# Kernel tuning notes

Measured on AMD Instinct MI355X. Metric: run time of the kernel, lower is better.

## Reference

```python
import jax, jax.numpy as jnp
import numpy as np

VOCAB, EMB, HID = 32000, 256, 512
B, S = 4, 512


def setup_inputs() -> dict:
    key = jax.random.key(0)
    ks = jax.random.split(key, 8)
    sc_e = 1.0  # torch nn.Embedding default: N(0,1)
    k_lstm = 1.0 / np.sqrt(HID)
    k_lin = 1.0 / np.sqrt(HID)
    emb = jax.random.normal(ks[0], (VOCAB, EMB), dtype=jnp.float32) * sc_e
    emb = emb.at[0].set(0.0)  # padding_idx=0 row is zero
    w_ih = jax.random.uniform(ks[1], (4 * HID, EMB), minval=-k_lstm, maxval=k_lstm)
    w_hh = jax.random.uniform(ks[2], (4 * HID, HID), minval=-k_lstm, maxval=k_lstm)
    b_ih = jax.random.uniform(ks[3], (4 * HID,), minval=-k_lstm, maxval=k_lstm)
    b_hh = jax.random.uniform(ks[4], (4 * HID,), minval=-k_lstm, maxval=k_lstm)
    W = jax.random.uniform(ks[5], (VOCAB, HID), minval=-k_lin, maxval=k_lin)
    b = jax.random.uniform(ks[6], (VOCAB,), minval=-k_lin, maxval=k_lin)
    batch = jax.random.randint(ks[7], (B, S), 0, VOCAB, dtype=jnp.int64 if jax.config.jax_enable_x64 else jnp.int32)
    return {"batch": batch, "emb": emb, "w_ih": w_ih, "w_hh": w_hh,
            "b_ih": b_ih, "b_hh": b_hh, "W": W, "b": b}


def _lstm(x, w_ih, w_hh, b_ih, b_hh):
    # x: [B, S, E]; torch gate order i, f, g, o; h0 = c0 = 0
    H = w_hh.shape[1]
    bsz = x.shape[0]
    xp = jnp.einsum('bse,ge->bsg', x, w_ih) + b_ih + b_hh  # [B,S,4H]
    xp = jnp.swapaxes(xp, 0, 1)  # [S,B,4H]

    def step(carry, xt):
        h, c = carry
        g = xt + h @ w_hh.T
        i, f, gg, o = jnp.split(g, 4, axis=-1)
        i, f, o = jax.nn.sigmoid(i), jax.nn.sigmoid(f), jax.nn.sigmoid(o)
        c = f * c + i * jnp.tanh(gg)
        h = o * jnp.tanh(c)
        return (h, c), h

    h0 = jnp.zeros((bsz, H), x.dtype)
    _, hs = jax.lax.scan(step, (h0, h0), xp)
    return jnp.swapaxes(hs, 0, 1)  # [B,S,H]


def reference(batch, emb, w_ih, w_hh, b_ih, b_hh, W, b):
    embeds = emb[batch]                               # [B,S,E]
    lstm_out = _lstm(embeds, w_ih, w_hh, b_ih, b_hh)  # [B,S,H]
    logits = jnp.einsum('bsh,vh->bsv', lstm_out, W) + b
    scores = jax.nn.log_softmax(logits, axis=2)       # [B,S,V]
    # Faithful to torch: contiguous view (row-major reinterpretation)
    V = W.shape[0]
    bsz = batch.shape[0]
    scores2 = scores.reshape(-1, V, bsz)              # [S,V,B]
    tgt2 = batch.reshape(-1, bsz)                     # [S,B]
    picked = jnp.take_along_axis(scores2, tgt2[:, None, :], axis=1)[:, 0, :]
    return -jnp.mean(picked)
```

## Files before the change

kernel.cpp:

```cpp
#include <hip/hip_runtime.h>
#include <hip/hip_bf16.h>
#include <math.h>

#define VOCAB 32000
#define EMB   256
#define HID   512
#define BB    4
#define SS    512
#define G4H   2048
#define BS    2048

typedef unsigned int   u32;
typedef unsigned short u16;
using short8 = __attribute__((ext_vector_type(8))) short;
using f32x4  = __attribute__((ext_vector_type(4))) float;

#define OFF_HSB  8192000ull
#define OFF_HW   8716288ull
#define OFF_SUM  8722432ull

__device__ inline unsigned packbf(float a, float b) {
    unsigned ua = __float_as_uint(a), ub = __float_as_uint(b);
    ua += 0x7fffu + ((ua >> 16) & 1u);
    ub += 0x7fffu + ((ub >> 16) & 1u);
    return (ua >> 16) | (ub & 0xffff0000u);
}

__device__ inline float lo16(unsigned w) { return __uint_as_float(w << 16); }
__device__ inline float hi16(unsigned w) { return __uint_as_float(w & 0xffff0000u); }

__device__ inline float fast_tanh(float x) {
    return 1.f - 2.f / (__expf(2.f * x) + 1.f);
}

#define GLOAD_LDS16(gp, lp) __builtin_amdgcn_global_load_lds( \
    (const __attribute__((address_space(1))) void*)(gp),      \
    (__attribute__((address_space(3))) void*)(lp), 16, 0, 0)

__global__ __launch_bounds__(256) void k_embed_xp(
    const int* __restrict__ batch, const float* __restrict__ emb,
    const float* __restrict__ w_ih, const float* __restrict__ b_ih,
    const float* __restrict__ b_hh, float* __restrict__ xp)
{
    __shared__ float Asl[16 * 64];
    __shared__ float Bsl[16 * 64];
    const int tid = threadIdx.x;
    const int bs0 = blockIdx.x * 64;
    const int g0  = blockIdx.y * 64;
    const int m  = tid & 63;
    const int kg = tid >> 6;
    const int tok = batch[bs0 + m];
    const float* arow = emb + (size_t)tok * EMB;
    const float* brow = w_ih + (size_t)(g0 + m) * EMB;
    const int tm = tid >> 4;
    const int tv = tid & 15;

    float acc[4][4] = {};
    for (int k0 = 0; k0 < EMB; k0 += 16) {
        float4 a4 = *(const float4*)(arow + k0 + kg * 4);
        float4 b4 = *(const float4*)(brow + k0 + kg * 4);
        __syncthreads();
        const int kb = kg * 4;
        Asl[(kb + 0) * 64 + m] = a4.x;
        Asl[(kb + 1) * 64 + m] = a4.y;
        Asl[(kb + 2) * 64 + m] = a4.z;
        Asl[(kb + 3) * 64 + m] = a4.w;
        Bsl[(kb + 0) * 64 + m] = b4.x;
        Bsl[(kb + 1) * 64 + m] = b4.y;
        Bsl[(kb + 2) * 64 + m] = b4.z;
        Bsl[(kb + 3) * 64 + m] = b4.w;
        __syncthreads();
#pragma unroll
        for (int k = 0; k < 16; ++k) {
            float4 av = *(const float4*)&Asl[k * 64 + tm * 4];
            float4 bv = *(const float4*)&Bsl[k * 64 + tv * 4];
            float a[4] = {av.x, av.y, av.z, av.w};
            float bb[4] = {bv.x, bv.y, bv.z, bv.w};
#pragma unroll
            for (int i = 0; i < 4; ++i)
#pragma unroll
                for (int j = 0; j < 4; ++j)
                    acc[i][j] += a[i] * bb[j];
        }
    }
    float bsum[4];
#pragma unroll
    for (int j = 0; j < 4; ++j) {
        int g = g0 + tv * 4 + j;
        bsum[j] = b_ih[g] + b_hh[g];
    }
    const int cg = g0 + tv * 4;
    const int gg = cg >> 9;
    const int jj = cg & 511;
    const int sl = jj >> 5;
    const int li = jj & 31;
#pragma unroll
    for (int i = 0; i < 4; ++i) {
        int row = bs0 + tm * 4 + i;
        int cch = row >> 9, tt = row & 511;
        float4 o;
        o.x = acc[i][0] + bsum[0];
        o.y = acc[i][1] + bsum[1];
        o.z = acc[i][2] + bsum[2];
        o.w = acc[i][3] + bsum[3];
        *(float4*)(xp + ((size_t)(cch * 16 + sl) * SS + tt) * 128 +
                   gg * 32 + li) = o;
    }
}

__global__ __launch_bounds__(512) void k_lstm(
    const float* __restrict__ w_hh, const float* __restrict__ xp2,
    u32* __restrict__ hw, u16* __restrict__ hsaveB)
{
    __shared__ float hl[4 * 132];
    __shared__ float gacc[128];

    const int tid   = threadIdx.x;
    const int wg    = blockIdx.x;
    const int c     = wg >> 4;
    const int slice = wg & 15;
    const int j0    = slice * 32;
    const int r     = tid >> 2;
    const int q     = tid & 3;
    const int grow  = (r >> 5) * HID + j0 + (r & 31);

    unsigned wreg[64];
    {
        const float* wsrc = w_hh + (size_t)grow * HID + q * 128;
#pragma unroll
        for (int i = 0; i < 32; ++i) {
            float4 f = *(const float4*)(wsrc + i * 4);
            wreg[2 * i]     = packbf(f.x, f.y);
            wreg[2 * i + 1] = packbf(f.z, f.w);
        }
    }

    const float* xbase = xp2 + (size_t)(c * 16 + slice) * (SS * 128) + r;
    float cst = 0.f;

    for (int t = 0; t < SS; ++t) {
        const int p = t & 1;
        float xsv = xbase[t * 128];
        u32 w;
        {
            u32* addr = hw + p * (BB * HID) + c * HID + tid;
            int guard = 0;
            for (;;) {
                w = __hip_atomic_load(addr, __ATOMIC_RELAXED,
                                      __HIP_MEMORY_SCOPE_AGENT);
                if ((w & 0xffffu) == (u32)t) break;
                __builtin_amdgcn_s_sleep(1);
                if (++guard > 2000000) break;
            }
        }
        hl[(tid >> 7) * 132 + (tid & 127)] = __uint_as_float(w & 0xffff0000u);
        __syncthreads();

        float a0 = 0.f, a1 = 0.f, a2 = 0.f, a3 = 0.f;
        {
            const float4* h4 = (const float4*)&hl[q * 132];
#pragma unroll
            for (int k = 0; k < 32; k += 4) {
                float4 v0 = h4[k + 0];
                unsigned wa = wreg[2 * k + 0], wb = wreg[2 * k + 1];
                a0 = fmaf(v0.x, lo16(wa), a0);
                a0 = fmaf(v0.y, hi16(wa), a0);
                a0 = fmaf(v0.z, lo16(wb), a0);
                a0 = fmaf(v0.w, hi16(wb), a0);
                float4 v1 = h4[k + 1];
                wa = wreg[2 * k + 2]; wb = wreg[2 * k + 3];
                a1 = fmaf(v1.x, lo16(wa), a1);
                a1 = fmaf(v1.y, hi16(wa), a1);
                a1 = fmaf(v1.z, lo16(wb), a1);
                a1 = fmaf(v1.w, hi16(wb), a1);
                float4 v2 = h4[k + 2];
                wa = wreg[2 * k + 4]; wb = wreg[2 * k + 5];
                a2 = fmaf(v2.x, lo16(wa), a2);
                a2 = fmaf(v2.y, hi16(wa), a2);
                a2 = fmaf(v2.z, lo16(wb), a2);
                a2 = fmaf(v2.w, hi16(wb), a2);
                float4 v3 = h4[k + 3];
                wa = wreg[2 * k + 6]; wb = wreg[2 * k + 7];
                a3 = fmaf(v3.x, lo16(wa), a3);
                a3 = fmaf(v3.y, hi16(wa), a3);
                a3 = fmaf(v3.z, lo16(wb), a3);
                a3 = fmaf(v3.w, hi16(wb), a3);
            }
        }
        float acc = (a0 + a1) + (a2 + a3);
        acc += __shfl_xor(acc, 1);
        acc += __shfl_xor(acc, 2);
        if (q == 0) gacc[r] = acc + xsv;
        __syncthreads();

        if (tid < 32) {
            float iv = gacc[tid],      fv = gacc[32 + tid];
            float gv = gacc[64 + tid], ov = gacc[96 + tid];
            float si = 1.f / (1.f + __expf(-iv));
            float sf = 1.f / (1.f + __expf(-fv));
            float so = 1.f / (1.f + __expf(-ov));
            cst = sf * cst + si * fast_tanh(gv);
            float hv = so * fast_tanh(cst);
            unsigned uu = __float_as_uint(hv);
            uu += 0x7fffu + ((uu >> 16) & 1u);
            uu &= 0xffff0000u;
            __hip_atomic_store(hw + (p ^ 1) * (BB * HID) + c * HID + j0 + tid,
                               uu | (u32)(t + 1), __ATOMIC_RELAXED,
                               __HIP_MEMORY_SCOPE_AGENT);
            hsaveB[(size_t)(c * SS + t) * HID + j0 + tid] = (u16)(uu >> 16);
        }
    }
}

__global__ __launch_bounds__(256) void k_wcvt(
    const float* __restrict__ W, u16* __restrict__ WB)
{
    int i = blockIdx.x * 256 + threadIdx.x;
    float4 f = ((const float4*)W)[i];
    uint2 o;
    o.x = packbf(f.x, f.y);
    o.y = packbf(f.z, f.w);
    ((uint2*)WB)[i] = o;
}

__global__ __launch_bounds__(256) void k_logits_lse(
    const u16* __restrict__ hsaveB, const u16* __restrict__ WB,
    const float* __restrict__ bias, float* __restrict__ sumexp)
{
    __shared__ u16 As[128 * 64];
    __shared__ u16 Bs[128 * 64];
    const int tid  = threadIdx.x;
    const int lane = tid & 63;
    const int wave = tid >> 6;
    const int wr   = wave >> 1;
    const int wc   = wave & 1;
    const int bs0  = blockIdx.x * 128;
    const int v0   = blockIdx.y * 128;
    const int lr   = lane & 15;
    const int lc   = lane >> 4;

    f32x4 acc[4][4];
#pragma unroll
    for (int m = 0; m < 4; ++m)
#pragma unroll
        for (int n = 0; n < 4; ++n)
            acc[m][n] = (f32x4){0.f, 0.f, 0.f, 0.f};

    for (int k0 = 0; k0 < HID; k0 += 64) {
#pragma unroll
        for (int it = 0; it < 4; ++it) {
            int base = it * 256 + wave * 64;
            int idx  = base + lane;
            int row  = idx >> 3, cl = idx & 7;
            int gcl  = cl ^ (row & 7);
            const u16* gA = hsaveB + (size_t)(bs0 + row) * HID + k0 + gcl * 8;
            GLOAD_LDS16(gA, As + (size_t)base * 8);
            const u16* gB = WB + (size_t)(v0 + row) * HID + k0 + gcl * 8;
            GLOAD_LDS16(gB, Bs + (size_t)base * 8);
        }
        asm volatile("s_waitcnt vmcnt(0)" ::: "memory");
        __syncthreads();

        short8 af[4][2], bf[4][2];
#pragma unroll
        for (int m = 0; m < 4; ++m)
#pragma unroll
            for (int ks = 0; ks < 2; ++ks) {
                int rowA = wr * 64 + m * 16 + lr;
                int swa  = ((ks * 4 + lc) ^ (rowA & 7)) * 8;
                af[m][ks] = *(const short8*)&As[rowA * 64 + swa];
                int rowB = wc * 64 + m * 16 + lr;
                int swb  = ((ks * 4 + lc) ^ (rowB & 7)) * 8;
                bf[m][ks] = *(const short8*)&Bs[rowB * 64 + swb];
            }
#pragma unroll
        for (int m = 0; m < 4; ++m)
#pragma unroll
            for (int n = 0; n < 4; ++n)
#pragma unroll
                for (int ks = 0; ks < 2; ++ks)
                    acc[m][n] = __builtin_amdgcn_mfma_f32_16x16x32_bf16(
                        af[m][ks], bf[n][ks], acc[m][n], 0, 0, 0);
        __syncthreads();
    }

    float bn[4];
#pragma unroll
    for (int n = 0; n < 4; ++n)
        bn[n] = bias[v0 + wc * 64 + n * 16 + lr];

#pragma unroll
    for (int m = 0; m < 4; ++m) {
        float p0 = 0.f, p1 = 0.f, p2 = 0.f, p3 = 0.f;
#pragma unroll
        for (int n = 0; n < 4; ++n) {
            float b = bn[n];
            p0 += __expf(acc[m][n][0] + b);
            p1 += __expf(acc[m][n][1] + b);
            p2 += __expf(acc[m][n][2] + b);
            p3 += __expf(acc[m][n][3] + b);
        }
#pragma unroll
        for (int off = 1; off < 16; off <<= 1) {
            p0 += __shfl_xor(p0, off);
            p1 += __shfl_xor(p1, off);
            p2 += __shfl_xor(p2, off);
            p3 += __shfl_xor(p3, off);
        }
        if (lr == 0) {
            int row = bs0 + wr * 64 + m * 16 + lc * 4;
            atomicAdd(&sumexp[row + 0], p0);
            atomicAdd(&sumexp[row + 1], p1);
            atomicAdd(&sumexp[row + 2], p2);
            atomicAdd(&sumexp[row + 3], p3);
        }
    }
}

__device__ inline float dotp(u32 h, u32 w) {
    return __uint_as_float(h << 16) * __uint_as_float(w << 16) +
           __uint_as_float(h & 0xffff0000u) * __uint_as_float(w & 0xffff0000u);
}

__global__ __launch_bounds__(256) void k_final(
    const int* __restrict__ batch, const u16* __restrict__ hsaveB,
    const u16* __restrict__ WB, const float* __restrict__ bias,
    const float* __restrict__ sumexp, float* __restrict__ out)
{
    const int gt   = blockIdx.x * 256 + threadIdx.x;
    const int wid  = gt >> 6;
    const int lane = gt & 63;
    const unsigned tgt = (unsigned)batch[wid];
    const unsigned s2 = wid >> 2, b2 = wid & 3;
    const unsigned j = s2 * (VOCAB * BB) + tgt * BB + b2;
    const unsigned SV = (unsigned)SS * VOCAB;
    const unsigned b_o = j / SV;
    const unsigned rr = j - b_o * SV;
    const unsigned s_o = rr / VOCAB;
    const unsigned v_o = rr - s_o * VOCAB;
    const unsigned row = b_o * SS + s_o;

    uint4 hu = *(const uint4*)(hsaveB + (size_t)row * HID + lane * 8);
    uint4 wu = *(const uint4*)(WB + (size_t)v_o * HID + lane * 8);
    float d = dotp(hu.x, wu.x) + dotp(hu.y, wu.y) +
              dotp(hu.z, wu.z) + dotp(hu.w, wu.w);
#pragma unroll
    for (int off = 32; off >= 1; off >>= 1)
        d += __shfl_xor(d, off);
    if (lane == 0) {
        float picked = d + bias[v_o] - logf(sumexp[row]);
        atomicAdd(out, -picked * (1.f / (float)BS));
    }
}

extern "C" void kernel_launch(void* const* d_in, const int* in_sizes, int n_in,
                              void* d_out, int out_size, void* d_ws, size_t ws_size,
                              hipStream_t stream)
{
    const int*   batch = (const int*)d_in[0];
    const float* emb   = (const float*)d_in[1];
    const float* w_ih  = (const float*)d_in[2];
    const float* w_hh  = (const float*)d_in[3];
    const float* b_ih  = (const float*)d_in[4];
    const float* b_hh  = (const float*)d_in[5];
    const float* Wm    = (const float*)d_in[6];
    const float* bvec  = (const float*)d_in[7];
    float* out = (float*)d_out;
    float* ws  = (float*)d_ws;

    float* xp      = ws;
    u16*   WB      = (u16*)ws;
    u16*   hsaveB  = (u16*)(ws + OFF_HSB);
    u32*   hw      = (u32*)(ws + OFF_HW);
    float* sumexp  = ws + OFF_SUM;

    hipMemsetAsync(hw, 0, (4096 + 2048 + 2048) * sizeof(float), stream);
    hipMemsetAsync(out, 0, sizeof(float), stream);

    dim3 g1(BS / 64, G4H / 64);
    k_embed_xp<<<g1, 256, 0, stream>>>(batch, emb, w_ih, b_ih, b_hh, xp);

    k_lstm<<<64, 512, 0, stream>>>(w_hh, xp, hw, hsaveB);

    k_wcvt<<<VOCAB * HID / 4 / 256, 256, 0, stream>>>(Wm, WB);

    dim3 g3(BS / 128, VOCAB / 128);
    k_logits_lse<<<g3, 256, 0, stream>>>(hsaveB, WB, bvec, sumexp);

    k_final<<<BS * 64 / 256, 256, 0, stream>>>(batch, hsaveB, WB, bvec, sumexp, out);
}
```

Before: 1.145 ms.

## Fuse LSTM and logits GEMM into one persistent kernel with progress flags

Merges the recurrent LSTM kernel and the logits/log-sum-exp GEMM into a single launch. 64 blocks run the recurrence and publish per-slice progress every 128 timesteps. 500 additional blocks wait on those flags and compute 128x256 logit tiles for completed time chunks, so the vocab GEMM overlaps with the serial recurrence. The separate W-to-bf16 conversion kernel is removed: W is read as fp32 and converted on the fly inside the GEMM tile load and in the final kernel. This adds spin-wait polling, relies on all 564 blocks being co-resident, and doubles fp32 W traffic in the GEMM.

```diff
diff --git a/kernel.cpp b/kernel.cpp
--- a/kernel.cpp
+++ b/kernel.cpp
@@ -9,6 +9,8 @@
 #define SS    512
 #define G4H   2048
 #define BS    2048
+#define NLSTM 64
+#define NW    500
 
 typedef unsigned int   u32;
 typedef unsigned short u16;
@@ -17,6 +19,7 @@
 
 #define OFF_HSB  8192000ull
 #define OFF_HW   8716288ull
+#define OFF_PRG  8720384ull
 #define OFF_SUM  8722432ull
 
 __device__ inline unsigned packbf(float a, float b) {
@@ -108,223 +111,259 @@
     }
 }
 
-__global__ __launch_bounds__(512) void k_lstm(
+__global__ __launch_bounds__(512) void k_fused(
     const float* __restrict__ w_hh, const float* __restrict__ xp2,
-    u32* __restrict__ hw, u16* __restrict__ hsaveB)
+    u32* __restrict__ hw, u32* __restrict__ prog, u16* __restrict__ hsaveB,
+    const float* __restrict__ Wm, const float* __restrict__ bias,
+    float* __restrict__ sumexp)
 {
+    __shared__ u16 As[128 * 64];
+    __shared__ u16 Bs[256 * 64];
     __shared__ float hl[4 * 132];
     __shared__ float gacc[128];
 
-    const int tid   = threadIdx.x;
-    const int wg    = blockIdx.x;
-    const int c     = wg >> 4;
-    const int slice = wg & 15;
-    const int j0    = slice * 32;
-    const int r     = tid >> 2;
-    const int q     = tid & 3;
-    const int grow  = (r >> 5) * HID + j0 + (r & 31);
-
-    unsigned wreg[64];
-    {
-        const float* wsrc = w_hh + (size_t)grow * HID + q * 128;
-#pragma unroll
-        for (int i = 0; i < 32; ++i) {
-            float4 f = *(const float4*)(wsrc + i * 4);
-            wreg[2 * i]     = packbf(f.x, f.y);
-            wreg[2 * i + 1] = packbf(f.z, f.w);
+    const int bid = blockIdx.x;
+    const int tid = threadIdx.x;
+
+    if (bid < NLSTM) {
+        const int c     = bid >> 4;
+        const int slice = bid & 15;
+        const int j0    = slice * 32;
+        const int r     = tid >> 2;
+        const int q     = tid & 3;
+        const int grow  = (r >> 5) * HID + j0 + (r & 31);
+
+        unsigned wreg[64];
+        {
+            const float* wsrc = w_hh + (size_t)grow * HID + q * 128;
+#pragma unroll
+            for (int i = 0; i < 32; ++i) {
+                float4 f = *(const float4*)(wsrc + i * 4);
+                wreg[2 * i]     = packbf(f.x, f.y);
+                wreg[2 * i + 1] = packbf(f.z, f.w);
+            }
         }
-    }
-
-    const float* xbase = xp2 + (size_t)(c * 16 + slice) * (SS * 128) + r;
-    float cst = 0.f;
-
-    for (int t = 0; t < SS; ++t) {
-        const int p = t & 1;
-        float xsv = xbase[t * 128];
-        u32 w;
-        {
-            u32* addr = hw + p * (BB * HID) + c * HID + tid;
-            int guard = 0;
-            for (;;) {
-                w = __hip_atomic_load(addr, __ATOMIC_RELAXED,
-                                      __HIP_MEMORY_SCOPE_AGENT);
-                if ((w & 0xffffu) == (u32)t) break;
-                __builtin_amdgcn_s_sleep(1);
-                if (++guard > 2000000) break;
+
+        const float* xbase = xp2 + (size_t)(c * 16 + slice) * (SS * 128) + r;
+        float cst = 0.f;
+
+        for (int t = 0; t < SS; ++t) {
+            const int p = t & 1;
+            float xsv = xbase[t * 128];
+            u32 w;
+            {
+                u32* addr = hw + p * (BB * HID) + c * HID + tid;
+                int guard = 0;
+                for (;;) {
+                    w = __hip_atomic_load(addr, __ATOMIC_RELAXED,
+                                          __HIP_MEMORY_SCOPE_AGENT);
+                    if ((w & 0xffffu) == (u32)t) break;
+                    __builtin_amdgcn_s_sleep(1);
+                    if (++guard > 2000000) break;
+                }
+            }
+            hl[(tid >> 7) * 132 + (tid & 127)] =
+                __uint_as_float(w & 0xffff0000u);
+            __syncthreads();
+
+            float a0 = 0.f, a1 = 0.f, a2 = 0.f, a3 = 0.f;
+            {
+                const float4* h4 = (const float4*)&hl[q * 132];
+#pragma unroll
+                for (int k = 0; k < 32; k += 4) {
+                    float4 v0 = h4[k + 0];
+                    unsigned wa = wreg[2 * k + 0], wb = wreg[2 * k + 1];
+                    a0 = fmaf(v0.x, lo16(wa), a0);
+                    a0 = fmaf(v0.y, hi16(wa), a0);
+                    a0 = fmaf(v0.z, lo16(wb), a0);
+                    a0 = fmaf(v0.w, hi16(wb), a0);
+                    float4 v1 = h4[k + 1];
+                    wa = wreg[2 * k + 2]; wb = wreg[2 * k + 3];
+                    a1 = fmaf(v1.x, lo16(wa), a1);
+                    a1 = fmaf(v1.y, hi16(wa), a1);
+                    a1 = fmaf(v1.z, lo16(wb), a1);
+                    a1 = fmaf(v1.w, hi16(wb), a1);
+                    float4 v2 = h4[k + 2];
+                    wa = wreg[2 * k + 4]; wb = wreg[2 * k + 5];
+                    a2 = fmaf(v2.x, lo16(wa), a2);
+                    a2 = fmaf(v2.y, hi16(wa), a2);
+                    a2 = fmaf(v2.z, lo16(wb), a2);
+                    a2 = fmaf(v2.w, hi16(wb), a2);
+                    float4 v3 = h4[k + 3];
+                    wa = wreg[2 * k + 6]; wb = wreg[2 * k + 7];
+                    a3 = fmaf(v3.x, lo16(wa), a3);
+                    a3 = fmaf(v3.y, hi16(wa), a3);
+                    a3 = fmaf(v3.z, lo16(wb), a3);
+                    a3 = fmaf(v3.w, hi16(wb), a3);
+                }
+            }
+            float acc = (a0 + a1) + (a2 + a3);
+            acc += __shfl_xor(acc, 1);
+            acc += __shfl_xor(acc, 2);
+            if (q == 0) gacc[r] = acc + xsv;
+            __syncthreads();
+
+            if (tid < 32) {
+                float iv = gacc[tid],      fv = gacc[32 + tid];
+                float gv = gacc[64 + tid], ov = gacc[96 + tid];
+                float si = 1.f / (1.f + __expf(-iv));
+                float sf = 1.f / (1.f + __expf(-fv));
+                float so = 1.f / (1.f + __expf(-ov));
+                cst = sf * cst + si * fast_tanh(gv);
+                float hv = so * fast_tanh(cst);
+                unsigned uu = __float_as_uint(hv);
+                uu += 0x7fffu + ((uu >> 16) & 1u);
+                uu &= 0xffff0000u;
+                __hip_atomic_store(
+                    hw + (p ^ 1) * (BB * HID) + c * HID + j0 + tid,
+                    uu | (u32)(t + 1), __ATOMIC_RELAXED,
+                    __HIP_MEMORY_SCOPE_AGENT);
+                const u16* hsp = hsaveB + (size_t)(c * SS + t) * HID + j0 + tid;
+                u32 hval = uu >> 16;
+                asm volatile("global_store_short %0, %1, off sc0 sc1"
+                             :: "v"(hsp), "v"(hval) : "memory");
+            }
+            if (((t + 1) & 127) == 0) {
+                if (tid < 64)
+                    asm volatile("s_waitcnt vmcnt(0)" ::: "memory");
+                if (tid == 0)
+                    __hip_atomic_store(&prog[c * 16 + slice], (u32)(t + 1),
+                                       __ATOMIC_RELAXED,
+                                       __HIP_MEMORY_SCOPE_AGENT);
             }
         }
-        hl[(tid >> 7) * 132 + (tid & 127)] = __uint_as_float(w & 0xffff0000u);
-        __syncthreads();
-
-        float a0 = 0.f, a1 = 0.f, a2 = 0.f, a3 = 0.f;
-        {
-            const float4* h4 = (const float4*)&hl[q * 132];
-#pragma unroll
-            for (int k = 0; k < 32; k += 4) {
-                float4 v0 = h4[k + 0];
-                unsigned wa = wreg[2 * k + 0], wb = wreg[2 * k + 1];
-                a0 = fmaf(v0.x, lo16(wa), a0);
-                a0 = fmaf(v0.y, hi16(wa), a0);
-                a0 = fmaf(v0.z, lo16(wb), a0);
-                a0 = fmaf(v0.w, hi16(wb), a0);
-                float4 v1 = h4[k + 1];
-                wa = wreg[2 * k + 2]; wb = wreg[2 * k + 3];
-                a1 = fmaf(v1.x, lo16(wa), a1);
-                a1 = fmaf(v1.y, hi16(wa), a1);
-                a1 = fmaf(v1.z, lo16(wb), a1);
-                a1 = fmaf(v1.w, hi16(wb), a1);
-                float4 v2 = h4[k + 2];
-                wa = wreg[2 * k + 4]; wb = wreg[2 * k + 5];
-                a2 = fmaf(v2.x, lo16(wa), a2);
-                a2 = fmaf(v2.y, hi16(wa), a2);
-                a2 = fmaf(v2.z, lo16(wb), a2);
-                a2 = fmaf(v2.w, hi16(wb), a2);
-                float4 v3 = h4[k + 3];
-                wa = wreg[2 * k + 6]; wb = wreg[2 * k + 7];
-                a3 = fmaf(v3.x, lo16(wa), a3);
-                a3 = fmaf(v3.y, hi16(wa), a3);
-                a3 = fmaf(v3.z, lo16(wb), a3);
-                a3 = fmaf(v3.w, hi16(wb), a3);
-            }
-        }
-        float acc = (a0 + a1) + (a2 + a3);
-        acc += __shfl_xor(acc, 1);
-        acc += __shfl_xor(acc, 2);
-        if (q == 0) gacc[r] = acc + xsv;
-        __syncthreads();
-
-        if (tid < 32) {
-            float iv = gacc[tid],      fv = gacc[32 + tid];
-            float gv = gacc[64 + tid], ov = gacc[96 + tid];
-            float si = 1.f / (1.f + __expf(-iv));
-            float sf = 1.f / (1.f + __expf(-fv));
-            float so = 1.f / (1.f + __expf(-ov));
-            cst = sf * cst + si * fast_tanh(gv);
-            float hv = so * fast_tanh(cst);
-            unsigned uu = __float_as_uint(hv);
-            uu += 0x7fffu + ((uu >> 16) & 1u);
-            uu &= 0xffff0000u;
-            __hip_atomic_store(hw + (p ^ 1) * (BB * HID) + c * HID + j0 + tid,
-                               uu | (u32)(t + 1), __ATOMIC_RELAXED,
-                               __HIP_MEMORY_SCOPE_AGENT);
-            hsaveB[(size_t)(c * SS + t) * HID + j0 + tid] = (u16)(uu >> 16);
-        }
-    }
-}
-
-__global__ __launch_bounds__(256) void k_wcvt(
-    const float* __restrict__ W, u16* __restrict__ WB)
-{
-    int i = blockIdx.x * 256 + threadIdx.x;
-    float4 f = ((const float4*)W)[i];
-    uint2 o;
-    o.x = packbf(f.x, f.y);
-    o.y = packbf(f.z, f.w);
-    ((uint2*)WB)[i] = o;
-}
-
-__global__ __launch_bounds__(256) void k_logits_lse(
-    const u16* __restrict__ hsaveB, const u16* __restrict__ WB,
-    const float* __restrict__ bias, float* __restrict__ sumexp)
-{
-    __shared__ u16 As[128 * 64];
-    __shared__ u16 Bs[128 * 64];
-    const int tid  = threadIdx.x;
+        return;
+    }
+
+    const int w    = bid - NLSTM;
     const int lane = tid & 63;
     const int wave = tid >> 6;
-    const int wr   = wave >> 1;
-    const int wc   = wave & 1;
-    const int bs0  = blockIdx.x * 128;
-    const int v0   = blockIdx.y * 128;
+    const int wr   = wave >> 2;
+    const int wc   = wave & 3;
     const int lr   = lane & 15;
     const int lc   = lane >> 4;
 
-    f32x4 acc[4][4];
-#pragma unroll
-    for (int m = 0; m < 4; ++m)
-#pragma unroll
-        for (int n = 0; n < 4; ++n)
-            acc[m][n] = (f32x4){0.f, 0.f, 0.f, 0.f};
-
-    for (int k0 = 0; k0 < HID; k0 += 64) {
-#pragma unroll
-        for (int it = 0; it < 4; ++it) {
-            int base = it * 256 + wave * 64;
-            int idx  = base + lane;
-            int row  = idx >> 3, cl = idx & 7;
-            int gcl  = cl ^ (row & 7);
-            const u16* gA = hsaveB + (size_t)(bs0 + row) * HID + k0 + gcl * 8;
-            GLOAD_LDS16(gA, As + (size_t)base * 8);
-            const u16* gB = WB + (size_t)(v0 + row) * HID + k0 + gcl * 8;
-            GLOAD_LDS16(gB, Bs + (size_t)base * 8);
+    for (int r = 0; r < 4; ++r) {
+        const u32 target = (u32)((r + 1) * 128);
+        for (int j = w; j < 500; j += NW) {
+            const int c   = j / 125;
+            const int vt  = j - c * 125;
+            const int bs0 = c * 512 + r * 128;
+            const int v0  = vt * 256;
+
+            if (tid < 16) {
+                int guard = 0;
+                for (;;) {
+                    u32 pv = __hip_atomic_load(&prog[c * 16 + tid],
+                                               __ATOMIC_RELAXED,
+                                               __HIP_MEMORY_SCOPE_AGENT);
+                    if (pv >= target) break;
+                    __builtin_amdgcn_s_sleep(127);
+                    __builtin_amdgcn_s_sleep(127);
+                    __builtin_amdgcn_s_sleep(127);
+                    if (++guard > 300000) break;
+                }
+            }
+            __syncthreads();
+
+            f32x4 acc[4][4];
+#pragma unroll
+            for (int m = 0; m < 4; ++m)
+#pragma unroll
+                for (int n = 0; n < 4; ++n)
+                    acc[m][n] = (f32x4){0.f, 0.f, 0.f, 0.f};
+
+            for (int k0 = 0; k0 < HID; k0 += 64) {
+#pragma unroll
+                for (int it = 0; it < 2; ++it) {
+                    int base = it * 512 + wave * 64;
+                    int idx  = base + lane;
+                    int row  = idx >> 3, cl = idx & 7;
+                    int gcl  = cl ^ (row & 7);
+                    const u16* gA = hsaveB + (size_t)(bs0 + row) * HID +
+                                    k0 + gcl * 8;
+                    GLOAD_LDS16(gA, As + (size_t)base * 8);
+                }
+#pragma unroll
+                for (int it = 0; it < 4; ++it) {
+                    int idx = it * 512 + tid;
+                    int row = idx >> 3, l = idx & 7;
+                    int g   = l ^ (row & 7);
+                    const float* src = Wm + (size_t)(v0 + row) * HID +
+                                       k0 + g * 8;
+                    float4 f0 = *(const float4*)src;
+                    float4 f1 = *(const float4*)(src + 4);
+                    uint4 pk;
+                    pk.x = packbf(f0.x, f0.y);
+                    pk.y = packbf(f0.z, f0.w);
+                    pk.z = packbf(f1.x, f1.y);
+                    pk.w = packbf(f1.z, f1.w);
+                    *(uint4*)&Bs[row * 64 + l * 8] = pk;
+                }
+                asm volatile("s_waitcnt vmcnt(0)" ::: "memory");
+                __syncthreads();
+
+                short8 af[4][2], bf[4][2];
+#pragma unroll
+                for (int m = 0; m < 4; ++m)
+#pragma unroll
+                    for (int ks = 0; ks < 2; ++ks) {
+                        int rowA = wr * 64 + m * 16 + lr;
+                        int swa  = ((ks * 4 + lc) ^ (rowA & 7)) * 8;
+                        af[m][ks] = *(const short8*)&As[rowA * 64 + swa];
+                        int rowB = wc * 64 + m * 16 + lr;
+                        int swb  = ((ks * 4 + lc) ^ (rowB & 7)) * 8;
+                        bf[m][ks] = *(const short8*)&Bs[rowB * 64 + swb];
+                    }
+#pragma unroll
+                for (int m = 0; m < 4; ++m)
+#pragma unroll
+                    for (int n = 0; n < 4; ++n)
+#pragma unroll
+                        for (int ks = 0; ks < 2; ++ks)
+                            acc[m][n] = __builtin_amdgcn_mfma_f32_16x16x32_bf16(
+                                af[m][ks], bf[n][ks], acc[m][n], 0, 0, 0);
+                __syncthreads();
+            }
+
+            float bn[4];
+#pragma unroll
+            for (int n = 0; n < 4; ++n)
+                bn[n] = bias[v0 + wc * 64 + n * 16 + lr];
+
+#pragma unroll
+            for (int m = 0; m < 4; ++m) {
+                float p0 = 0.f, p1 = 0.f, p2 = 0.f, p3 = 0.f;
+#pragma unroll
+                for (int n = 0; n < 4; ++n) {
+                    float b = bn[n];
+                    p0 += __expf(acc[m][n][0] + b);
+                    p1 += __expf(acc[m][n][1] + b);
+                    p2 += __expf(acc[m][n][2] + b);
+                    p3 += __expf(acc[m][n][3] + b);
+                }
+#pragma unroll
+                for (int off = 1; off < 16; off <<= 1) {
+                    p0 += __shfl_xor(p0, off);
+                    p1 += __shfl_xor(p1, off);
+                    p2 += __shfl_xor(p2, off);
+                    p3 += __shfl_xor(p3, off);
+                }
+                if (lr == 0) {
+                    int row = bs0 + wr * 64 + m * 16 + lc * 4;
+                    atomicAdd(&sumexp[row + 0], p0);
+                    atomicAdd(&sumexp[row + 1], p1);
+                    atomicAdd(&sumexp[row + 2], p2);
+                    atomicAdd(&sumexp[row + 3], p3);
+                }
+            }
         }
-        asm volatile("s_waitcnt vmcnt(0)" ::: "memory");
-        __syncthreads();
-
-        short8 af[4][2], bf[4][2];
-#pragma unroll
-        for (int m = 0; m < 4; ++m)
-#pragma unroll
-            for (int ks = 0; ks < 2; ++ks) {
-                int rowA = wr * 64 + m * 16 + lr;
-                int swa  = ((ks * 4 + lc) ^ (rowA & 7)) * 8;
-                af[m][ks] = *(const short8*)&As[rowA * 64 + swa];
-                int rowB = wc * 64 + m * 16 + lr;
-                int swb  = ((ks * 4 + lc) ^ (rowB & 7)) * 8;
-                bf[m][ks] = *(const short8*)&Bs[rowB * 64 + swb];
-            }
-#pragma unroll
-        for (int m = 0; m < 4; ++m)
-#pragma unroll
-            for (int n = 0; n < 4; ++n)
-#pragma unroll
-                for (int ks = 0; ks < 2; ++ks)
-                    acc[m][n] = __builtin_amdgcn_mfma_f32_16x16x32_bf16(
-                        af[m][ks], bf[n][ks], acc[m][n], 0, 0, 0);
-        __syncthreads();
-    }
-
-    float bn[4];
-#pragma unroll
-    for (int n = 0; n < 4; ++n)
-        bn[n] = bias[v0 + wc * 64 + n * 16 + lr];
-
-#pragma unroll
-    for (int m = 0; m < 4; ++m) {
-        float p0 = 0.f, p1 = 0.f, p2 = 0.f, p3 = 0.f;
-#pragma unroll
-        for (int n = 0; n < 4; ++n) {
-            float b = bn[n];
-            p0 += __expf(acc[m][n][0] + b);
-            p1 += __expf(acc[m][n][1] + b);
-            p2 += __expf(acc[m][n][2] + b);
-            p3 += __expf(acc[m][n][3] + b);
-        }
-#pragma unroll
-        for (int off = 1; off < 16; off <<= 1) {
-            p0 += __shfl_xor(p0, off);
-            p1 += __shfl_xor(p1, off);
-            p2 += __shfl_xor(p2, off);
-            p3 += __shfl_xor(p3, off);
-        }
-        if (lr == 0) {
-            int row = bs0 + wr * 64 + m * 16 + lc * 4;
-            atomicAdd(&sumexp[row + 0], p0);
-            atomicAdd(&sumexp[row + 1], p1);
-            atomicAdd(&sumexp[row + 2], p2);
-            atomicAdd(&sumexp[row + 3], p3);
-        }
-    }
-}
-
-__device__ inline float dotp(u32 h, u32 w) {
-    return __uint_as_float(h << 16) * __uint_as_float(w << 16) +
-           __uint_as_float(h & 0xffff0000u) * __uint_as_float(w & 0xffff0000u);
+    }
 }
 
 __global__ __launch_bounds__(256) void k_final(
     const int* __restrict__ batch, const u16* __restrict__ hsaveB,
-    const u16* __restrict__ WB, const float* __restrict__ bias,
+    const float* __restrict__ Wm, const float* __restrict__ bias,
     const float* __restrict__ sumexp, float* __restrict__ out)
 {
     const int gt   = blockIdx.x * 256 + threadIdx.x;
@@ -341,9 +380,13 @@
     const unsigned row = b_o * SS + s_o;
 
     uint4 hu = *(const uint4*)(hsaveB + (size_t)row * HID + lane * 8);
-    uint4 wu = *(const uint4*)(WB + (size_t)v_o * HID + lane * 8);
-    float d = dotp(hu.x, wu.x) + dotp(hu.y, wu.y) +
-              dotp(hu.z, wu.z) + dotp(hu.w, wu.w);
+    const float* wp = Wm + (size_t)v_o * HID + lane * 8;
+    float4 w0 = *(const float4*)wp;
+    float4 w1 = *(const float4*)(wp + 4);
+    float d = lo16(hu.x) * w0.x + hi16(hu.x) * w0.y +
+              lo16(hu.y) * w0.z + hi16(hu.y) * w0.w +
+              lo16(hu.z) * w1.x + hi16(hu.z) * w1.y +
+              lo16(hu.w) * w1.z + hi16(hu.w) * w1.w;
 #pragma unroll
     for (int off = 32; off >= 1; off >>= 1)
         d += __shfl_xor(d, off);
@@ -369,9 +412,9 @@
     float* ws  = (float*)d_ws;
 
     float* xp      = ws;
-    u16*   WB      = (u16*)ws;
     u16*   hsaveB  = (u16*)(ws + OFF_HSB);
     u32*   hw      = (u32*)(ws + OFF_HW);
+    u32*   prog    = (u32*)(ws + OFF_PRG);
     float* sumexp  = ws + OFF_SUM;
 
     hipMemsetAsync(hw, 0, (4096 + 2048 + 2048) * sizeof(float), stream);
@@ -380,12 +423,9 @@
     dim3 g1(BS / 64, G4H / 64);
     k_embed_xp<<<g1, 256, 0, stream>>>(batch, emb, w_ih, b_ih, b_hh, xp);
 
-    k_lstm<<<64, 512, 0, stream>>>(w_hh, xp, hw, hsaveB);
-
-    k_wcvt<<<VOCAB * HID / 4 / 256, 256, 0, stream>>>(Wm, WB);
-
-    dim3 g3(BS / 128, VOCAB / 128);
-    k_logits_lse<<<g3, 256, 0, stream>>>(hsaveB, WB, bvec, sumexp);
-
-    k_final<<<BS * 64 / 256, 256, 0, stream>>>(batch, hsaveB, WB, bvec, sumexp, out);
-}
+    k_fused<<<NLSTM + NW, 512, 0, stream>>>(w_hh, xp, hw, prog, hsaveB,
+                                            Wm, bvec, sumexp);
+
+    k_final<<<BS * 64 / 256, 256, 0, stream>>>(batch, hsaveB, Wm, bvec,
+                                               sumexp, out);
+}
```

Result: slower. 1.423 ms (+24.2%).
